# Kernel tuning notes

Measured on AMD Instinct MI355X. Metric: run time of the kernel, lower is better.

Reference implementation:

```python
import jax, jax.numpy as jnp
import numpy as np
import math

EMBED_DIM = 2048
NUM_HEADS = 32
NUM_KV_HEADS = 8
HEAD_DIM = EMBED_DIM // NUM_HEADS  # 64
N_REP = NUM_HEADS // NUM_KV_HEADS  # 4
BATCH = 2
SEQ = 2048


def _rope_tables(seq_len, head_dim):
    # standard RoPE tables matching rotate_half convention (frequencies tiled twice)
    inv_freq = 1.0 / (10000.0 ** (np.arange(0, head_dim, 2, dtype=np.float32) / head_dim))
    t = np.arange(seq_len, dtype=np.float32)
    freqs = np.outer(t, inv_freq)                      # (seq, head_dim/2)
    emb = np.concatenate([freqs, freqs], axis=-1)      # (seq, head_dim)
    return jnp.asarray(np.cos(emb)), jnp.asarray(np.sin(emb))


def setup_inputs() -> dict:
    key = jax.random.key(0)
    ks = jax.random.split(key, 6)
    scale = 1.0 / math.sqrt(EMBED_DIM)
    x = jax.random.normal(ks[0], (BATCH, SEQ, EMBED_DIM), dtype=jnp.float32)
    wq = jax.random.normal(ks[1], (EMBED_DIM, EMBED_DIM), dtype=jnp.float32) * scale
    wk = jax.random.normal(ks[2], (NUM_KV_HEADS * HEAD_DIM, EMBED_DIM), dtype=jnp.float32) * scale
    wv = jax.random.normal(ks[3], (NUM_KV_HEADS * HEAD_DIM, EMBED_DIM), dtype=jnp.float32) * scale
    wo = jax.random.normal(ks[4], (EMBED_DIM, EMBED_DIM), dtype=jnp.float32) * scale
    freqs_cos, freqs_sin = _rope_tables(SEQ, HEAD_DIM)
    return {"x": x, "freqs_cos": freqs_cos, "freqs_sin": freqs_sin,
            "wq": wq, "wk": wk, "wv": wv, "wo": wo}


def _rotate_half(t):
    h = t.shape[-1] // 2
    return jnp.concatenate([-t[..., h:], t[..., :h]], axis=-1)


def reference(x, freqs_cos, freqs_sin, wq, wk, wv, wo):
    b, s, _ = x.shape
    # QKV projections (Linear with weight (out,in): y = x @ W^T)
    xq = (x @ wq.T).reshape(b, s, NUM_HEADS, HEAD_DIM).transpose(0, 2, 1, 3)     # (b,H,s,d)
    xk = (x @ wk.T).reshape(b, s, NUM_KV_HEADS, HEAD_DIM).transpose(0, 2, 1, 3)  # (b,Hkv,s,d)
    xv = (x @ wv.T).reshape(b, s, NUM_KV_HEADS, HEAD_DIM).transpose(0, 2, 1, 3)
    # RoPE: cos/sin (s,d) broadcast over (b,h,s,d)
    xq = xq * freqs_cos + _rotate_half(xq) * freqs_sin
    xk = xk * freqs_cos + _rotate_half(xk) * freqs_sin
    # GQA: repeat_interleave kv heads to match q heads
    xk = jnp.repeat(xk, N_REP, axis=1)  # (b,H,s,d)
    xv = jnp.repeat(xv, N_REP, axis=1)
    scores = jnp.einsum('bhqd,bhkd->bhqk', xq, xk) / math.sqrt(HEAD_DIM)
    causal = jnp.tril(jnp.ones((s, s), dtype=bool))
    scores = jnp.where(causal, scores, jnp.float32(-1e30))
    attn = jax.nn.softmax(scores, axis=-1)
    out = jnp.einsum('bhqk,bhkd->bhqd', attn, xv)        # (b,H,s,d)
    out = out.transpose(0, 2, 1, 3).reshape(b, s, EMBED_DIM)
    return out @ wo.T
```

## Files before the change

kernel.cpp:

```cpp
#include <hip/hip_runtime.h>

#define BATCH 2
#define SEQ 2048
#define EMBED 2048
#define NHEADS 32
#define NKV 8
#define HDIM 64
#define QKV_LD 3072
#define LOG2E 1.44269504088896f

typedef __attribute__((ext_vector_type(8))) short short8;
typedef __attribute__((ext_vector_type(4))) float f32x4;

__device__ inline float hw_exp2(float x) { return __builtin_amdgcn_exp2f(x); }

__device__ inline ushort f2bf(float f) {
  union { float f; unsigned u; } v{f};
  unsigned r = v.u + 0x7FFF + ((v.u >> 16) & 1);
  return (ushort)(r >> 16);
}
__device__ inline float bf2f(ushort u) {
  union { unsigned u; float f; } v{((unsigned)u) << 16};
  return v.f;
}
__device__ inline unsigned fbits(float f) {
  union { float f; unsigned u; } v{f};
  return v.u;
}

__device__ inline void gload16(const ushort* g, ushort* l) {
  __builtin_amdgcn_global_load_lds(
      (const __attribute__((address_space(1))) unsigned*)g,
      (__attribute__((address_space(3))) unsigned*)l, 16, 0, 0);
}

#define PHASE_BAR()                          \
  do {                                       \
    __builtin_amdgcn_sched_barrier(0);       \
    __builtin_amdgcn_s_barrier();            \
    __builtin_amdgcn_sched_barrier(0);       \
  } while (0)

__global__ __launch_bounds__(256) void cvt_all(const float* __restrict__ x,
                                               const float* __restrict__ wq,
                                               const float* __restrict__ wk,
                                               const float* __restrict__ wv,
                                               const float* __restrict__ wo,
                                               ushort* __restrict__ xb,
                                               ushort* __restrict__ wqkv,
                                               ushort* __restrict__ wob) {
  size_t e = (size_t)(blockIdx.x * blockDim.x + threadIdx.x) * 8;
  const float* src;
  ushort* dst;
  if (e < 8388608u) { src = x + e; dst = xb + e; }
  else if (e < 12582912u) { size_t o = e - 8388608u; src = wq + o; dst = wqkv + o; }
  else if (e < 13631488u) { size_t o = e - 12582912u; src = wk + o; dst = wqkv + 4194304u + o; }
  else if (e < 14680064u) { size_t o = e - 13631488u; src = wv + o; dst = wqkv + 5242880u + o; }
  else { size_t o = e - 14680064u; src = wo + o; dst = wob + o; }
  float4 v0 = ((const float4*)src)[0];
  float4 v1 = ((const float4*)src)[1];
  union { uint4 v; ushort u[8]; } pk;
  pk.u[0] = f2bf(v0.x); pk.u[1] = f2bf(v0.y); pk.u[2] = f2bf(v0.z); pk.u[3] = f2bf(v0.w);
  pk.u[4] = f2bf(v1.x); pk.u[5] = f2bf(v1.y); pk.u[6] = f2bf(v1.z); pk.u[7] = f2bf(v1.w);
  *(uint4*)dst = pk.v;
}

template <int BN, int MODE, typename OutT>
__global__ __launch_bounds__(512) void gemm8p(const ushort* __restrict__ Ag,
                                              const ushort* __restrict__ Bg,
                                              OutT* __restrict__ C,
                                              const float* __restrict__ fc,
                                              const float* __restrict__ fs,
                                              int M, int N, int K) {
  constexpr int NF = BN / 64;
  __shared__ ushort As[2][2][256][32];
  __shared__ ushort Bs[2][2][BN][32];
  const int tid = threadIdx.x;
  const int lane = tid & 63, wave = tid >> 6;
  const int quad = lane >> 4, l16 = lane & 15;
  const int wm = wave >> 2, wn = wave & 3;
  const int m0 = blockIdx.y * 256, n0 = blockIdx.x * BN;
  const int NT = K >> 6;

  auto stA = [&](int Tn, int h) {
    const int r0 = h * 128 + wave * 16;
    const ushort* g = Ag + (size_t)(m0 + r0 + (lane >> 2)) * K + Tn * 64 + (lane & 3) * 8;
    gload16(g, &As[Tn & 1][0][r0][0]);
    gload16(g + 32, &As[Tn & 1][1][r0][0]);
  };
  auto stB = [&](int Tn, int h) {
    const int r0 = h * 128 + wave * 16;
    const ushort* g = Bg + (size_t)(n0 + r0 + (lane >> 2)) * K + Tn * 64 + (lane & 3) * 8;
    gload16(g, &Bs[Tn & 1][0][r0][0]);
    gload16(g + 32, &Bs[Tn & 1][1][r0][0]);
  };

  f32x4 acc[8][NF] = {};

  stA(0, 0); stA(0, 1);
  stB(0, 0);
  if constexpr (BN == 256) stB(0, 1);

  for (int T = 0; T < NT; ++T) {
    const int bf = T & 1;
    asm volatile("s_waitcnt vmcnt(0)" ::: "memory");
    PHASE_BAR();

    short8 bfr[NF][2];
#pragma unroll
    for (int nf = 0; nf < NF; nf++)
#pragma unroll
      for (int kk = 0; kk < 2; kk++)
        bfr[nf][kk] = *(short8*)&Bs[bf][kk][wn * (16 * NF) + nf * 16 + l16][quad * 8];

#pragma unroll
    for (int q = 0; q < 4; q++) {
      short8 afr[2][2];
#pragma unroll
      for (int mq = 0; mq < 2; mq++)
#pragma unroll
        for (int kk = 0; kk < 2; kk++)
          afr[mq][kk] = *(short8*)&As[bf][kk][wm * 128 + (2 * q + mq) * 16 + l16][quad * 8];

      if (T + 1 < NT) {
        if (q == 0) stA(T + 1, 0);
        else if (q == 1) stA(T + 1, 1);
        else if (q == 2) stB(T + 1, 0);
        else if constexpr (BN == 256) stB(T + 1, 1);
      }

      __builtin_amdgcn_s_setprio(1);
#pragma unroll
      for (int mq = 0; mq < 2; mq++)
#pragma unroll
        for (int nf = 0; nf < NF; nf++)
#pragma unroll
          for (int kk = 0; kk < 2; kk++)
            acc[2 * q + mq][nf] = __builtin_amdgcn_mfma_f32_16x16x32_bf16(
                afr[mq][kk], bfr[nf][kk], acc[2 * q + mq][nf], 0, 0, 0);
      __builtin_amdgcn_s_setprio(0);
      PHASE_BAR();
    }
  }

  if constexpr (MODE == 1) {
    if (n0 < 2560) {
      const float scale = (n0 < 2048) ? 0.125f * LOG2E : 1.0f;
      const int d0 = l16, d1 = l16 + 32;
      const int e0 = l16 + 16, e1 = l16 + 48;
#pragma unroll
      for (int mf = 0; mf < 8; mf++) {
#pragma unroll
        for (int r = 0; r < 4; r++) {
          size_t rg = (size_t)(m0 + wm * 128 + mf * 16 + quad * 4 + r);
          int s = (int)(rg & (SEQ - 1));
          const float* cb = fc + s * HDIM;
          const float* sb = fs + s * HDIM;
          float x0 = acc[mf][0][r], x2 = acc[mf][2][r];
          float y1 = acc[mf][1][r], y3 = acc[mf][3][r];
          float o0 = (x0 * cb[d0] - x2 * sb[d0]) * scale;
          float o2 = (x2 * cb[d1] + x0 * sb[d1]) * scale;
          float o1 = (y1 * cb[e0] - y3 * sb[e0]) * scale;
          float o3 = (y3 * cb[e1] + y1 * sb[e1]) * scale;
          ushort* Cr = (ushort*)C + rg * N + n0 + wn * 64 + l16;
          Cr[0]  = f2bf(o0);
          Cr[16] = f2bf(o1);
          Cr[32] = f2bf(o2);
          Cr[48] = f2bf(o3);
        }
      }
      return;
    }
  }
#pragma unroll
  for (int mf = 0; mf < 8; mf++) {
#pragma unroll
    for (int r = 0; r < 4; r++) {
      size_t rg = (size_t)(m0 + wm * 128 + mf * 16 + quad * 4 + r);
#pragma unroll
      for (int nf = 0; nf < NF; nf++) {
        int cg = n0 + wn * (16 * NF) + nf * 16 + l16;
        if constexpr (sizeof(OutT) == 2)
          C[rg * N + cg] = f2bf(acc[mf][nf][r]);
        else
          C[rg * N + cg] = acc[mf][nf][r];
      }
    }
  }
}

__global__ __launch_bounds__(256, 4) void attn_mfma(const ushort* __restrict__ QKV,
                                                    ushort* __restrict__ O) {
  __shared__ ushort Ks[64][72];
  __shared__ ushort Vt[64][72];
  __shared__ ushort Pw[4][16][72];
  const int tid = threadIdx.x;
  const int lane = tid & 63, wave = tid >> 6;
  const int quad = lane >> 4, l16 = lane & 15;

  const int bid = blockIdx.x;
  const int qq = bid >> 8;
  const int j4 = (bid >> 6) & 3;
  const int bh = bid & 63;
  const int qblk = (qq >> 1) * 8 + ((qq & 1) ? 7 - j4 : j4);

  const int b = bh >> 5, h = bh & 31, kh = h >> 2;
  const int ntiles = 2 * qblk + 2;
  const int wrow = qblk * 128 + wave * 32;

  short8 qf[2][2];
#pragma unroll
  for (int f = 0; f < 2; f++)
#pragma unroll
    for (int c = 0; c < 2; c++)
      qf[f][c] = *(const short8*)(QKV +
          (size_t)(b * SEQ + wrow + f * 16 + l16) * QKV_LD +
          h * HDIM + c * 32 + quad * 8);

  f32x4 o[2][4] = {};
  float m[2] = {-INFINITY, -INFINITY}, l[2] = {0.f, 0.f};

  const ushort* Kbase = QKV + (size_t)b * SEQ * QKV_LD + 2048 + kh * HDIM;
  const ushort* Vbase = Kbase + 512;
  const int kp = tid & 31, dg = tid >> 5;

  for (int t = 0; t < ntiles; t++) {
    const int k0 = t * 64;
    __syncthreads();
    {
      const float4* kpp = (const float4*)(Kbase + (size_t)(k0 + lane) * QKV_LD + wave * 16);
      float4 kv0 = kpp[0], kv1 = kpp[1];
      const uint4* va4 = (const uint4*)(Vbase + (size_t)(k0 + 2 * kp) * QKV_LD + dg * 8);
      const uint4* vb4 = (const uint4*)(Vbase + (size_t)(k0 + 2 * kp + 1) * QKV_LD + dg * 8);
      uint4 va = va4[0], vb = vb4[0];
      *(float4*)&Ks[lane][wave * 16] = kv0;
      *(float4*)&Ks[lane][wave * 16 + 8] = kv1;
      const unsigned* vaw = (const unsigned*)&va;
      const unsigned* vbw = (const unsigned*)&vb;
#pragma unroll
      for (int j = 0; j < 8; j++) {
        unsigned pk = (j & 1)
            ? __builtin_amdgcn_perm(vbw[j >> 1], vaw[j >> 1], 0x07060302)
            : __builtin_amdgcn_perm(vbw[j >> 1], vaw[j >> 1], 0x05040100);
        *(unsigned*)&Vt[dg * 8 + j][2 * kp] = pk;
      }
    }
    __syncthreads();

    if (k0 > wrow + 31) continue;
    const bool a0 = (k0 <= wrow + 15);

    f32x4 s0[4], s1[4];
    __builtin_amdgcn_s_setprio(1);
#pragma unroll
    for (int nt = 0; nt < 4; nt++) {
      short8 kf0 = *(short8*)&Ks[nt * 16 + l16][quad * 8];
      short8 kf1 = *(short8*)&Ks[nt * 16 + l16][32 + quad * 8];
      f32x4 z1 = {};
      z1 = __builtin_amdgcn_mfma_f32_16x16x32_bf16(kf0, qf[1][0], z1, 0, 0, 0);
      s1[nt] = __builtin_amdgcn_mfma_f32_16x16x32_bf16(kf1, qf[1][1], z1, 0, 0, 0);
      if (a0) {
        f32x4 z0 = {};
        z0 = __builtin_amdgcn_mfma_f32_16x16x32_bf16(kf0, qf[0][0], z0, 0, 0, 0);
        s0[nt] = __builtin_amdgcn_mfma_f32_16x16x32_bf16(kf1, qf[0][1], z0, 0, 0, 0);
      }
    }
    __builtin_amdgcn_s_setprio(0);

    if (k0 + 63 > wrow + 16) {
      const int lim1 = wrow + 16 + l16 - k0;
#pragma unroll
      for (int nt = 0; nt < 4; nt++)
#pragma unroll
        for (int r = 0; r < 4; r++)
          if (nt * 16 + quad * 4 + r > lim1) s1[nt][r] = -INFINITY;
    }
    if (a0 && k0 + 63 > wrow) {
      const int lim0 = wrow + l16 - k0;
#pragma unroll
      for (int nt = 0; nt < 4; nt++)
#pragma unroll
        for (int r = 0; r < 4; r++)
          if (nt * 16 + quad * 4 + r > lim0) s0[nt][r] = -INFINITY;
    }

    auto smx = [&](f32x4 (&s)[4], float& mm, float& ll, f32x4 (&oo)[4]) {
      float mx = s[0][0];
#pragma unroll
      for (int nt = 0; nt < 4; nt++)
#pragma unroll
        for (int r = 0; r < 4; r++) mx = fmaxf(mx, s[nt][r]);
      mx = fmaxf(mx, __shfl_xor(mx, 16));
      mx = fmaxf(mx, __shfl_xor(mx, 32));
      if (!__all(mx <= mm + 8.f)) {
        float mnew = fmaxf(mm, mx);
        float al = hw_exp2(mm - mnew);
        mm = mnew;
        ll *= al;
#pragma unroll
        for (int dt = 0; dt < 4; dt++)
#pragma unroll
          for (int r = 0; r < 4; r++) oo[dt][r] *= al;
      }
      float psum = 0.f;
#pragma unroll
      for (int nt = 0; nt < 4; nt++) {
        float p0 = hw_exp2(s[nt][0] - mm), p1 = hw_exp2(s[nt][1] - mm);
        float p2 = hw_exp2(s[nt][2] - mm), p3 = hw_exp2(s[nt][3] - mm);
        psum += (p0 + p1) + (p2 + p3);
        unsigned lo = __builtin_amdgcn_perm(fbits(p1), fbits(p0), 0x07060302);
        unsigned hi = __builtin_amdgcn_perm(fbits(p3), fbits(p2), 0x07060302);
        uint2 pk; pk.x = lo; pk.y = hi;
        *(uint2*)&Pw[wave][l16][nt * 16 + quad * 4] = pk;
      }
      psum += __shfl_xor(psum, 16);
      psum += __shfl_xor(psum, 32);
      ll += psum;
    };

    short8 pf00, pf01, pf10, pf11;
    if (a0) {
      smx(s0, m[0], l[0], o[0]);
      pf00 = *(short8*)&Pw[wave][l16][quad * 8];
      pf01 = *(short8*)&Pw[wave][l16][32 + quad * 8];
    }
    smx(s1, m[1], l[1], o[1]);
    pf10 = *(short8*)&Pw[wave][l16][quad * 8];
    pf11 = *(short8*)&Pw[wave][l16][32 + quad * 8];

    __builtin_amdgcn_s_setprio(1);
#pragma unroll
    for (int dt = 0; dt < 4; dt++) {
      short8 vf0 = *(short8*)&Vt[dt * 16 + l16][quad * 8];
      short8 vf1 = *(short8*)&Vt[dt * 16 + l16][32 + quad * 8];
      o[1][dt] = __builtin_amdgcn_mfma_f32_16x16x32_bf16(vf0, pf10, o[1][dt], 0, 0, 0);
      o[1][dt] = __builtin_amdgcn_mfma_f32_16x16x32_bf16(vf1, pf11, o[1][dt], 0, 0, 0);
      if (a0) {
        o[0][dt] = __builtin_amdgcn_mfma_f32_16x16x32_bf16(vf0, pf00, o[0][dt], 0, 0, 0);
        o[0][dt] = __builtin_amdgcn_mfma_f32_16x16x32_bf16(vf1, pf01, o[0][dt], 0, 0, 0);
      }
    }
    __builtin_amdgcn_s_setprio(0);
  }

#pragma unroll
  for (int f = 0; f < 2; f++) {
    float inv = 1.0f / l[f];
    size_t rowg = (size_t)(b * SEQ + wrow + f * 16 + l16) * EMBED + h * HDIM;
#pragma unroll
    for (int dt = 0; dt < 4; dt++) {
      ushort q0 = f2bf(o[f][dt][0] * inv), q1 = f2bf(o[f][dt][1] * inv);
      ushort q2 = f2bf(o[f][dt][2] * inv), q3 = f2bf(o[f][dt][3] * inv);
      uint2 pk;
      pk.x = (unsigned)q0 | ((unsigned)q1 << 16);
      pk.y = (unsigned)q2 | ((unsigned)q3 << 16);
      *(uint2*)&O[rowg + dt * 16 + quad * 4] = pk;
    }
  }
}

extern "C" void kernel_launch(void* const* d_in, const int* in_sizes, int n_in,
                              void* d_out, int out_size, void* d_ws, size_t ws_size,
                              hipStream_t stream) {
  const float* x = (const float*)d_in[0];
  const float* fcos = (const float*)d_in[1];
  const float* fsin = (const float*)d_in[2];
  const float* wq = (const float*)d_in[3];
  const float* wk = (const float*)d_in[4];
  const float* wv = (const float*)d_in[5];
  const float* wo = (const float*)d_in[6];
  float* out = (float*)d_out;

  const int M = BATCH * SEQ;
  ushort* ws = (ushort*)d_ws;
  ushort* xb = ws;
  ushort* wqkv = xb + (size_t)M * EMBED;
  ushort* wob = wqkv + (size_t)QKV_LD * EMBED;
  ushort* QKVb = wob + (size_t)EMBED * EMBED;
  ushort* Ab = QKVb + (size_t)M * QKV_LD;

  dim3 blk(256);
  cvt_all<<<9216, blk, 0, stream>>>(x, wq, wk, wv, wo, xb, wqkv, wob);

  gemm8p<256, 1, ushort><<<dim3(QKV_LD / 256, M / 256), dim3(512), 0, stream>>>(
      xb, wqkv, QKVb, fcos, fsin, M, QKV_LD, EMBED);

  attn_mfma<<<dim3(1024), blk, 0, stream>>>(QKVb, Ab);

  gemm8p<128, 0, float><<<dim3(EMBED / 128, M / 256), dim3(512), 0, stream>>>(
      Ab, wob, out, nullptr, nullptr, M, EMBED, EMBED);
}
```

Before: 317.4 us.

## Split long causal query blocks across two KV halves with a merge kernel

```diff
diff --git a/kernel.cpp b/kernel.cpp
--- a/kernel.cpp
+++ b/kernel.cpp
@@ -190,7 +190,9 @@
 }
 
 __global__ __launch_bounds__(256, 4) void attn_mfma(const ushort* __restrict__ QKV,
-                                                    ushort* __restrict__ O) {
+                                                    ushort* __restrict__ O,
+                                                    float* __restrict__ Opart,
+                                                    float* __restrict__ ml) {
   __shared__ ushort Ks[64][72];
   __shared__ ushort Vt[64][72];
   __shared__ ushort Pw[4][16][72];
@@ -199,13 +201,25 @@
   const int quad = lane >> 4, l16 = lane & 15;
 
   const int bid = blockIdx.x;
-  const int qq = bid >> 8;
-  const int j4 = (bid >> 6) & 3;
+  const int p = bid >> 6;
   const int bh = bid & 63;
-  const int qblk = (qq >> 1) * 8 + ((qq & 1) ? 7 - j4 : j4);
+  int qblk, t0, t1, half;
+  bool split;
+  if (p < 16) {
+    split = true;
+    half = p & 1;
+    qblk = 15 - (p >> 1);
+    t0 = half * (qblk + 1);
+    t1 = t0 + qblk + 1;
+  } else {
+    split = false;
+    half = 0;
+    qblk = 23 - p;
+    t0 = 0;
+    t1 = 2 * qblk + 2;
+  }
 
   const int b = bh >> 5, h = bh & 31, kh = h >> 2;
-  const int ntiles = 2 * qblk + 2;
   const int wrow = qblk * 128 + wave * 32;
 
   short8 qf[2][2];
@@ -224,7 +238,7 @@
   const ushort* Vbase = Kbase + 512;
   const int kp = tid & 31, dg = tid >> 5;
 
-  for (int t = 0; t < ntiles; t++) {
+  for (int t = t0; t < t1; t++) {
     const int k0 = t * 64;
     __syncthreads();
     {
@@ -343,20 +357,67 @@
     __builtin_amdgcn_s_setprio(0);
   }
 
-#pragma unroll
-  for (int f = 0; f < 2; f++) {
-    float inv = 1.0f / l[f];
-    size_t rowg = (size_t)(b * SEQ + wrow + f * 16 + l16) * EMBED + h * HDIM;
-#pragma unroll
-    for (int dt = 0; dt < 4; dt++) {
-      ushort q0 = f2bf(o[f][dt][0] * inv), q1 = f2bf(o[f][dt][1] * inv);
-      ushort q2 = f2bf(o[f][dt][2] * inv), q3 = f2bf(o[f][dt][3] * inv);
-      uint2 pk;
-      pk.x = (unsigned)q0 | ((unsigned)q1 << 16);
-      pk.y = (unsigned)q2 | ((unsigned)q3 << 16);
-      *(uint2*)&O[rowg + dt * 16 + quad * 4] = pk;
-    }
-  }
+  if (split) {
+    const int lrb = b * 1024 + (qblk - 8) * 128 + wave * 32;
+#pragma unroll
+    for (int f = 0; f < 2; f++) {
+      const int lr = lrb + f * 16 + l16;
+      if (quad == 0) {
+        float2* mlp = (float2*)ml + ((size_t)half * 2048 + lr) * 32 + h;
+        *mlp = make_float2(m[f], l[f]);
+      }
+      float* Op = Opart + ((size_t)half * 2048 + lr) * 2048 + h * 64;
+#pragma unroll
+      for (int dt = 0; dt < 4; dt++)
+        *(f32x4*)&Op[dt * 16 + quad * 4] = o[f][dt];
+    }
+  } else {
+#pragma unroll
+    for (int f = 0; f < 2; f++) {
+      float inv = 1.0f / l[f];
+      size_t rowg = (size_t)(b * SEQ + wrow + f * 16 + l16) * EMBED + h * HDIM;
+#pragma unroll
+      for (int dt = 0; dt < 4; dt++) {
+        ushort q0 = f2bf(o[f][dt][0] * inv), q1 = f2bf(o[f][dt][1] * inv);
+        ushort q2 = f2bf(o[f][dt][2] * inv), q3 = f2bf(o[f][dt][3] * inv);
+        uint2 pk;
+        pk.x = (unsigned)q0 | ((unsigned)q1 << 16);
+        pk.y = (unsigned)q2 | ((unsigned)q3 << 16);
+        *(uint2*)&O[rowg + dt * 16 + quad * 4] = pk;
+      }
+    }
+  }
+}
+
+__global__ __launch_bounds__(256) void attn_merge(const float* __restrict__ Opart,
+                                                  const float* __restrict__ ml,
+                                                  ushort* __restrict__ O) {
+  int idx = blockIdx.x * 256 + threadIdx.x;
+  int lr = idx >> 8;
+  int cg = (idx & 255) * 8;
+  int h = cg >> 6;
+  float2 ml0 = ((const float2*)ml)[((size_t)0 * 2048 + lr) * 32 + h];
+  float2 ml1 = ((const float2*)ml)[((size_t)1 * 2048 + lr) * 32 + h];
+  float M = fmaxf(ml0.x, ml1.x);
+  float a0 = hw_exp2(ml0.x - M), a1 = hw_exp2(ml1.x - M);
+  float inv = 1.0f / (ml0.y * a0 + ml1.y * a1);
+  const float4* p0 = (const float4*)(Opart + ((size_t)0 * 2048 + lr) * 2048 + cg);
+  const float4* p1 = (const float4*)(Opart + ((size_t)1 * 2048 + lr) * 2048 + cg);
+  float4 x0 = p0[0], x1 = p0[1];
+  float4 y0 = p1[0], y1 = p1[1];
+  union { uint4 v; ushort u[8]; } pk;
+  pk.u[0] = f2bf((x0.x * a0 + y0.x * a1) * inv);
+  pk.u[1] = f2bf((x0.y * a0 + y0.y * a1) * inv);
+  pk.u[2] = f2bf((x0.z * a0 + y0.z * a1) * inv);
+  pk.u[3] = f2bf((x0.w * a0 + y0.w * a1) * inv);
+  pk.u[4] = f2bf((x1.x * a0 + y1.x * a1) * inv);
+  pk.u[5] = f2bf((x1.y * a0 + y1.y * a1) * inv);
+  pk.u[6] = f2bf((x1.z * a0 + y1.z * a1) * inv);
+  pk.u[7] = f2bf((x1.w * a0 + y1.w * a1) * inv);
+  int b = lr >> 10;
+  int r = lr & 1023;
+  size_t grow = (size_t)b * SEQ + 1024 + r;
+  *(uint4*)&O[grow * EMBED + cg] = pk.v;
 }
 
 extern "C" void kernel_launch(void* const* d_in, const int* in_sizes, int n_in,
@@ -378,6 +439,8 @@
   ushort* wob = wqkv + (size_t)QKV_LD * EMBED;
   ushort* QKVb = wob + (size_t)EMBED * EMBED;
   ushort* Ab = QKVb + (size_t)M * QKV_LD;
+  float* Opart = (float*)(Ab + (size_t)M * EMBED);
+  float* mlbuf = Opart + (size_t)2 * 2048 * 2048;
 
   dim3 blk(256);
   cvt_all<<<9216, blk, 0, stream>>>(x, wq, wk, wv, wo, xb, wqkv, wob);
@@ -385,7 +448,8 @@
   gemm8p<256, 1, ushort><<<dim3(QKV_LD / 256, M / 256), dim3(512), 0, stream>>>(
       xb, wqkv, QKVb, fcos, fsin, M, QKV_LD, EMBED);
 
-  attn_mfma<<<dim3(1024), blk, 0, stream>>>(QKVb, Ab);
+  attn_mfma<<<dim3(1536), blk, 0, stream>>>(QKVb, Ab, Opart, mlbuf);
+  attn_merge<<<dim3(2048), blk, 0, stream>>>(Opart, mlbuf, Ab);
 
   gemm8p<128, 0, float><<<dim3(EMBED / 128, M / 256), dim3(512), 0, stream>>>(
       Ab, wob, out, nullptr, nullptr, M, EMBED, EMBED);
```

After: 326.8 us. 1.03x slower.
